# Kernel tuning notes

Hardware: AMD Instinct MI355X
Metric: run time of the kernel (lower is better)

## Reference

```python
import jax, jax.numpy as jnp
import numpy as np

D_MODEL = 1024
N_HEADS = 16
HEAD_DIM = D_MODEL // N_HEADS


def setup_inputs() -> dict:
    key = jax.random.key(0)
    ks = jax.random.split(key, 12)
    B, L = 2, 2048
    s = 1.0 / np.sqrt(D_MODEL)
    inp = {
        "q": jax.random.normal(ks[0], (B, L, D_MODEL), dtype=jnp.float32),
        "k": jax.random.normal(ks[1], (B, L, D_MODEL), dtype=jnp.float32),
        "v": jax.random.normal(ks[2], (B, L, D_MODEL), dtype=jnp.float32),
        "mask": jax.random.randint(ks[3], (B, L), 0, 2).astype(jnp.bool_),
        "Wq": jax.random.normal(ks[4], (D_MODEL, D_MODEL), dtype=jnp.float32) * s,
        "bq": jnp.zeros((D_MODEL,), dtype=jnp.float32),
        "Wk": jax.random.normal(ks[5], (D_MODEL, D_MODEL), dtype=jnp.float32) * s,
        "bk": jnp.zeros((D_MODEL,), dtype=jnp.float32),
        "Wv": jax.random.normal(ks[6], (D_MODEL, D_MODEL), dtype=jnp.float32) * s,
        "bv": jnp.zeros((D_MODEL,), dtype=jnp.float32),
        "Wo": jax.random.normal(ks[7], (D_MODEL, D_MODEL), dtype=jnp.float32) * s,
        "bo": jnp.zeros((D_MODEL,), dtype=jnp.float32),
    }
    return inp


def reference(q, k, v, mask, Wq, bq, Wk, bk, Wv, bv, Wo, bo):
    B, Lq, _ = q.shape
    Lk = k.shape[1]
    # torch Linear: y = x @ W.T + b; W is [out, in]
    Q = (jnp.einsum("bld,ed->ble", q, Wq) + bq).reshape(B, Lq, N_HEADS, HEAD_DIM).transpose(0, 2, 1, 3)
    K = (jnp.einsum("bld,ed->ble", k, Wk) + bk).reshape(B, Lk, N_HEADS, HEAD_DIM).transpose(0, 2, 1, 3)
    V = (jnp.einsum("bld,ed->ble", v, Wv) + bv).reshape(B, Lk, N_HEADS, HEAD_DIM).transpose(0, 2, 1, 3)
    scale = 1.0 / np.sqrt(HEAD_DIM).astype(np.float32)
    scores = jnp.einsum("bhqd,bhkd->bhqk", Q, K) * scale  # [B,H,Lq,Lk]
    # mask: True = masked out; broadcast (B,1,1,Lk)
    scores = jnp.where(mask[:, None, None, :], -jnp.inf, scores)
    attn = jax.nn.softmax(scores, axis=-1)
    out = jnp.einsum("bhqk,bhkd->bhqd", attn, V)  # [B,H,Lq,hd]
    out = out.transpose(0, 2, 1, 3).reshape(B, Lq, D_MODEL)
    return jnp.einsum("bld,ed->ble", out, Wo) + bo
```

## Files before the change

### kernel.cpp

```cpp
#include <hip/hip_runtime.h>

typedef unsigned short u16;
typedef __bf16 bf16x8 __attribute__((ext_vector_type(8)));
typedef float f32x4 __attribute__((ext_vector_type(4)));
typedef unsigned int u32x4 __attribute__((ext_vector_type(4)));
typedef unsigned int u32x2 __attribute__((ext_vector_type(2)));

#define MFMA16(a, b, c) __builtin_amdgcn_mfma_f32_16x16x32_bf16((a), (b), (c), 0, 0, 0)

__device__ __forceinline__ u16 f2bf(float f) {
    unsigned u = __builtin_bit_cast(unsigned, f);
    u = u + 0x7FFFu + ((u >> 16) & 1u);
    return (u16)(u >> 16);
}
__device__ __forceinline__ unsigned pk2(float a, float b) {
    return (unsigned)f2bf(a) | ((unsigned)f2bf(b) << 16);
}
__device__ __forceinline__ u32x4 pk8(f32x4 a, f32x4 b) {
    u32x4 r;
    r[0] = pk2(a[0], a[1]); r[1] = pk2(a[2], a[3]);
    r[2] = pk2(b[0], b[1]); r[3] = pk2(b[2], b[3]);
    return r;
}
__device__ __forceinline__ unsigned pkhu(float a, float b) {
    unsigned ua = __builtin_bit_cast(unsigned, a) + 0x8000u;
    unsigned ub = __builtin_bit_cast(unsigned, b) + 0x8000u;
    return __builtin_amdgcn_perm(ub, ua, 0x07060302u);
}
__device__ __forceinline__ float exp2_fast(float x) {
    float r;
    asm("v_exp_f32 %0, %1" : "=v"(r) : "v"(x));
    return r;
}
__device__ __forceinline__ void lds_load16(const u16* g, u16* l) {
    __builtin_amdgcn_global_load_lds(
        (const __attribute__((address_space(1))) void*)g,
        (__attribute__((address_space(3))) void*)l, 16, 0, 0);
}

#define QSCALE 0.18033688011112042f
#define FIXMAX 13.0f

__global__ __launch_bounds__(256) void convert_bf16(
    const float* __restrict__ q, const float* __restrict__ k, const float* __restrict__ v,
    const float* __restrict__ Wq, const float* __restrict__ Wk, const float* __restrict__ Wv,
    const float* __restrict__ Wo, u16* __restrict__ dst)
{
    const size_t i = ((size_t)blockIdx.x * 256 + threadIdx.x) * 8;
    const size_t QE = 4194304, WE = 1048576;
    const float* s;
    if (i < QE) s = q + i;
    else if (i < 2 * QE) s = k + (i - QE);
    else if (i < 3 * QE) s = v + (i - 2 * QE);
    else {
        size_t j = i - 3 * QE;
        if (j < WE) s = Wq + j;
        else if (j < 2 * WE) s = Wk + (j - WE);
        else if (j < 3 * WE) s = Wv + (j - 2 * WE);
        else s = Wo + (j - 3 * WE);
    }
    f32x4 a = *(const f32x4*)s;
    f32x4 b = *(const f32x4*)(s + 4);
    *(u32x4*)(dst + i) = pk8(a, b);
}

__device__ __forceinline__ void gemm128_core64(
    const u16* __restrict__ A, const u16* __restrict__ B,
    int m0, int n0, u16* As, u16* Bs, int tid, f32x4 acc[4][4])
{
    const int wv = tid >> 6, lane = tid & 63, quad = lane >> 4, l16 = lane & 15;
    const int mh = (wv >> 1) * 64, nh = (wv & 1) * 64;

    int rr[4], gc[4];
    u16 *ldsA[4], *ldsB[4];
    #pragma unroll
    for (int i = 0; i < 4; i++) {
        const int sbase = wv * 64 + i * 256;
        const int seg = sbase + lane;
        rr[i] = seg >> 3;
        const int c = seg & 7;
        gc[i] = c ^ (rr[i] & 7);
        ldsA[i] = As + sbase * 8;
        ldsB[i] = Bs + sbase * 8;
    }
    const u16* gA = A + (size_t)m0 * 1024;
    const u16* gB = B + (size_t)n0 * 1024;

    for (int t = 0; t < 16; t++) {
        const int k0 = t * 64;
        __syncthreads();
        #pragma unroll
        for (int i = 0; i < 4; i++)
            lds_load16(gA + (size_t)rr[i] * 1024 + k0 + gc[i] * 8, ldsA[i]);
        #pragma unroll
        for (int i = 0; i < 4; i++)
            lds_load16(gB + (size_t)rr[i] * 1024 + k0 + gc[i] * 8, ldsB[i]);
        __syncthreads();
        #pragma unroll
        for (int hf = 0; hf < 2; hf++) {
            bf16x8 af[4], bfr[4];
            #pragma unroll
            for (int mi = 0; mi < 4; mi++)
                af[mi] = *(const bf16x8*)&As[(mh + mi * 16 + l16) * 64 +
                                            (((quad + 4 * hf) ^ (l16 & 7)) * 8)];
            #pragma unroll
            for (int ni = 0; ni < 4; ni++)
                bfr[ni] = *(const bf16x8*)&Bs[(nh + ni * 16 + l16) * 64 +
                                              (((quad + 4 * hf) ^ (l16 & 7)) * 8)];
            #pragma unroll
            for (int mi = 0; mi < 4; mi++)
                #pragma unroll
                for (int ni = 0; ni < 4; ni++)
                    acc[mi][ni] = MFMA16(af[mi], bfr[ni], acc[mi][ni]);
        }
    }
}

__global__ __launch_bounds__(256) void qkv_bf(
    const u16* __restrict__ qb, const u16* __restrict__ kb, const u16* __restrict__ vb,
    const u16* __restrict__ wq, const u16* __restrict__ wk, const u16* __restrict__ wvv,
    const float* __restrict__ bq, const float* __restrict__ bk, const float* __restrict__ bv,
    u16* __restrict__ Qh, u16* __restrict__ Kh, u16* __restrict__ Vt)
{
    __shared__ alignas(16) u16 As[128 * 64];
    __shared__ alignas(16) u16 Bs[128 * 64];
    const int z = blockIdx.z;
    const u16* A = (z == 0) ? qb : (z == 1) ? kb : vb;
    const u16* B = (z == 0) ? wq : (z == 1) ? wk : wvv;
    const float* bias = (z == 0) ? bq : (z == 1) ? bk : bv;
    const int tid = threadIdx.x;
    const int m0 = blockIdx.y * 128, n0 = blockIdx.x * 128;
    const int wv = tid >> 6, lane = tid & 63, quad = lane >> 4, l16 = lane & 15;
    const int mh = (wv >> 1) * 64, nh = (wv & 1) * 64;

    f32x4 acc[4][4];
    #pragma unroll
    for (int i = 0; i < 4; i++)
        #pragma unroll
        for (int j = 0; j < 4; j++) acc[i][j] = (f32x4){0.f, 0.f, 0.f, 0.f};

    gemm128_core64(A, B, m0, n0, As, Bs, tid, acc);

    const float scl = (z == 0) ? QSCALE : 1.0f;
    u16* outp = (z == 0) ? Qh : (z == 1) ? Kh : Vt;
    #pragma unroll
    for (int ni = 0; ni < 4; ni++) {
        const int n = n0 + nh + ni * 16 + l16;
        const float bval = bias[n];
        const int h = n >> 6, d = n & 63;
        #pragma unroll
        for (int mi = 0; mi < 4; mi++) {
            const int mbase = m0 + mh + mi * 16 + quad * 4;
            #pragma unroll
            for (int r = 0; r < 4; r++) {
                const int m = mbase + r;
                const int bb = m >> 11, l = m & 2047;
                const float val = (acc[mi][ni][r] + bval) * scl;
                size_t idx;
                if (z < 2) idx = (((size_t)(bb * 16 + h) * 2048 + l) << 6) + d;
                else       idx = (((size_t)(bb * 16 + h) * 64 + d) << 11) + l;
                outp[idx] = f2bf(val);
            }
        }
    }
}

__global__ __launch_bounds__(256) void out_bf(
    const u16* __restrict__ Ob, const u16* __restrict__ wo,
    const float* __restrict__ bo, float* __restrict__ out)
{
    __shared__ alignas(16) u16 As[128 * 64];
    __shared__ alignas(16) u16 Bs[128 * 64];
    const int tid = threadIdx.x;
    const int m0 = blockIdx.y * 128, n0 = blockIdx.x * 128;
    const int wv = tid >> 6, lane = tid & 63, quad = lane >> 4, l16 = lane & 15;
    const int mh = (wv >> 1) * 64, nh = (wv & 1) * 64;

    f32x4 acc[4][4];
    #pragma unroll
    for (int i = 0; i < 4; i++)
        #pragma unroll
        for (int j = 0; j < 4; j++) acc[i][j] = (f32x4){0.f, 0.f, 0.f, 0.f};

    gemm128_core64(Ob, wo, m0, n0, As, Bs, tid, acc);

    #pragma unroll
    for (int ni = 0; ni < 4; ni++) {
        const int n = n0 + nh + ni * 16 + l16;
        const float bval = bo[n];
        #pragma unroll
        for (int mi = 0; mi < 4; mi++) {
            const int mbase = m0 + mh + mi * 16 + quad * 4;
            #pragma unroll
            for (int r = 0; r < 4; r++)
                out[(size_t)(mbase + r) * 1024 + n] = acc[mi][ni][r] + bval;
        }
    }
}

__global__ __launch_bounds__(256) void attn3(
    const u16* __restrict__ Qh, const u16* __restrict__ Kh,
    const u16* __restrict__ Vt, const int* __restrict__ mask,
    u16* __restrict__ Ob)
{
    __shared__ alignas(16) u16 Ks[2][64 * 72];
    __shared__ alignas(16) u16 Vs[2][64 * 72];
    __shared__ alignas(16) u16 Ps[4][16 * 72];
    __shared__ alignas(16) float Ms[2][64];

    const int tid = threadIdx.x;
    const int blk = blockIdx.x;
    const int bh = blk & 31, qt = blk >> 5;
    const int b = bh >> 4, h = bh & 15;
    const int wv = tid >> 6, lane = tid & 63, quad = lane >> 4, l16 = lane & 15;

    const int qbase = qt * 128 + wv * 32;
    const u16* Qb = Qh + ((size_t)bh * 2048 + qbase) * 64;
    bf16x8 qf[2][2];
    #pragma unroll
    for (int sub = 0; sub < 2; sub++)
        #pragma unroll
        for (int hf = 0; hf < 2; hf++)
            qf[sub][hf] = *(const bf16x8*)(Qb + (sub * 16 + l16) * 64 + hf * 32 + quad * 8);

    const u16* Kb = Kh + (size_t)bh * 2048 * 64;
    const u16* Vb = Vt + (size_t)bh * 64 * 2048;
    const int* mb = mask + b * 2048;

    const int s0 = tid, s1 = tid + 256;
    const int r0 = s0 >> 3, c0 = (s0 & 7) * 8;
    const int r1 = s1 >> 3, c1 = (s1 & 7) * 8;

    u32x4 rk0 = *(const u32x4*)(Kb + r0 * 64 + c0);
    u32x4 rk1 = *(const u32x4*)(Kb + r1 * 64 + c1);
    u32x4 rv0 = *(const u32x4*)(Vb + (size_t)r0 * 2048 + c0);
    u32x4 rv1 = *(const u32x4*)(Vb + (size_t)r1 * 2048 + c1);
    float rm = (tid < 64) ? (mb[tid] ? -1e30f : -FIXMAX) : 0.f;

    f32x4 o[2][4];
    #pragma unroll
    for (int sub = 0; sub < 2; sub++)
        #pragma unroll
        for (int db = 0; db < 4; db++) o[sub][db] = (f32x4){0.f, 0.f, 0.f, 0.f};
    float Lrun[2] = {0.f, 0.f};

    for (int kc = 0; kc < 32; kc++) {
        const int bi = kc & 1;
        u16* KsB = Ks[bi];
        u16* VsB = Vs[bi];
        *(u32x4*)&KsB[r0 * 72 + c0] = rk0;
        *(u32x4*)&KsB[r1 * 72 + c1] = rk1;
        *(u32x4*)&VsB[r0 * 72 + c0] = rv0;
        *(u32x4*)&VsB[r1 * 72 + c1] = rv1;
        if (tid < 64) Ms[bi][tid] = rm;
        __syncthreads();

        if (kc < 31) {
            const int off = (kc + 1) * 64;
            rk0 = *(const u32x4*)(Kb + (size_t)(off + r0) * 64 + c0);
            rk1 = *(const u32x4*)(Kb + (size_t)(off + r1) * 64 + c1);
            rv0 = *(const u32x4*)(Vb + (size_t)r0 * 2048 + off + c0);
            rv1 = *(const u32x4*)(Vb + (size_t)r1 * 2048 + off + c1);
            rm = (tid < 64) ? (mb[off + tid] ? -1e30f : -FIXMAX) : 0.f;
        }

        f32x4 mneg[4];
        #pragma unroll
        for (int nb = 0; nb < 4; nb++)
            mneg[nb] = *(const f32x4*)&Ms[bi][nb * 16 + quad * 4];

        #pragma unroll
        for (int sub = 0; sub < 2; sub++) {
            f32x4 st[4];
            #pragma unroll
            for (int nb = 0; nb < 4; nb++) {
                const bf16x8 kf0 = *(const bf16x8*)&KsB[(nb * 16 + l16) * 72 + quad * 8];
                const bf16x8 kf1 = *(const bf16x8*)&KsB[(nb * 16 + l16) * 72 + 32 + quad * 8];
                f32x4 z = (f32x4){0.f, 0.f, 0.f, 0.f};
                z = MFMA16(kf0, qf[sub][0], z);
                z = MFMA16(kf1, qf[sub][1], z);
                st[nb] = z;
            }
            #pragma unroll
            for (int nb = 0; nb < 4; nb++) {
                st[nb] += mneg[nb];
                #pragma unroll
                for (int r = 0; r < 4; r++) st[nb][r] = exp2_fast(st[nb][r]);
            }
            f32x4 s4 = st[0] + st[1] + st[2] + st[3];
            float sm = (s4[0] + s4[1]) + (s4[2] + s4[3]);
            sm += __shfl_xor(sm, 16, 64);
            sm += __shfl_xor(sm, 32, 64);
            Lrun[sub] += sm;

            u16* prow = &Ps[wv][l16 * 72];
            #pragma unroll
            for (int nb = 0; nb < 4; nb++) {
                u32x2 w;
                w[0] = pkhu(st[nb][0], st[nb][1]);
                w[1] = pkhu(st[nb][2], st[nb][3]);
                *(u32x2*)&prow[nb * 16 + quad * 4] = w;
            }

            asm volatile("s_waitcnt lgkmcnt(0)" ::: "memory");

            const bf16x8 pf0 = *(const bf16x8*)&Ps[wv][l16 * 72 + quad * 8];
            const bf16x8 pf1 = *(const bf16x8*)&Ps[wv][l16 * 72 + 32 + quad * 8];
            #pragma unroll
            for (int db = 0; db < 4; db++) {
                const bf16x8 vf0 = *(const bf16x8*)&VsB[(db * 16 + l16) * 72 + quad * 8];
                const bf16x8 vf1 = *(const bf16x8*)&VsB[(db * 16 + l16) * 72 + 32 + quad * 8];
                o[sub][db] = MFMA16(pf0, vf0, o[sub][db]);
                o[sub][db] = MFMA16(pf1, vf1, o[sub][db]);
            }
            asm volatile("" ::: "memory");
        }
    }

    #pragma unroll
    for (int sub = 0; sub < 2; sub++) {
        const float li = 1.0f / Lrun[sub];
        #pragma unroll
        for (int r = 0; r < 4; r++) {
            const float lr = __shfl(li, (lane & 48) | (quad * 4 + r), 64);
            const int qrow = qt * 128 + wv * 32 + sub * 16 + quad * 4 + r;
            #pragma unroll
            for (int db = 0; db < 4; db++)
                Ob[((size_t)(b * 2048 + qrow)) * 1024 + h * 64 + db * 16 + l16] =
                    f2bf(o[sub][db][r] * lr);
        }
    }
}

__global__ __launch_bounds__(256) void qkv_gemm(
    const float* __restrict__ q, const float* __restrict__ k, const float* __restrict__ v,
    const float* __restrict__ Wq, const float* __restrict__ Wk, const float* __restrict__ Wv,
    const float* __restrict__ bq, const float* __restrict__ bk, const float* __restrict__ bv,
    u16* __restrict__ Qh, u16* __restrict__ Kh, u16* __restrict__ Vt)
{
    __shared__ alignas(16) u16 As[128 * 40];
    __shared__ alignas(16) u16 Bs[128 * 40];
    const int z = blockIdx.z;
    const float* A    = (z == 0) ? q  : (z == 1) ? k  : v;
    const float* W    = (z == 0) ? Wq : (z == 1) ? Wk : Wv;
    const float* bias = (z == 0) ? bq : (z == 1) ? bk : bv;
    const int tid = threadIdx.x;
    const int m0 = blockIdx.y * 128, n0 = blockIdx.x * 128;
    const int row = tid >> 1, cseg = tid & 1;
    const float* ga = A + (size_t)(m0 + row) * 1024 + cseg * 16;
    const float* gb = W + (size_t)(n0 + row) * 1024 + cseg * 16;
    const int wv = tid >> 6, lane = tid & 63, quad = lane >> 4, l16 = lane & 15;
    const int mh = (wv >> 1) * 64, nh = (wv & 1) * 64;

    f32x4 acc[4][4];
    for (int i = 0; i < 4; i++)
        for (int j = 0; j < 4; j++) acc[i][j] = (f32x4){0.f, 0.f, 0.f, 0.f};

    f32x4 ra[4], rb[4];
    for (int i = 0; i < 4; i++) {
        ra[i] = *(const f32x4*)(ga + i * 4);
        rb[i] = *(const f32x4*)(gb + i * 4);
    }
    for (int t = 0; t < 32; t++) {
        __syncthreads();
        *(u32x4*)&As[row * 40 + cseg * 16]     = pk8(ra[0], ra[1]);
        *(u32x4*)&As[row * 40 + cseg * 16 + 8] = pk8(ra[2], ra[3]);
        *(u32x4*)&Bs[row * 40 + cseg * 16]     = pk8(rb[0], rb[1]);
        *(u32x4*)&Bs[row * 40 + cseg * 16 + 8] = pk8(rb[2], rb[3]);
        __syncthreads();
        if (t < 31) {
            const int k0 = (t + 1) * 32;
            for (int i = 0; i < 4; i++) {
                ra[i] = *(const f32x4*)(ga + k0 + i * 4);
                rb[i] = *(const f32x4*)(gb + k0 + i * 4);
            }
        }
        bf16x8 af[4], bfr[4];
        for (int mi = 0; mi < 4; mi++)
            af[mi] = *(const bf16x8*)&As[(mh + mi * 16 + l16) * 40 + quad * 8];
        for (int ni = 0; ni < 4; ni++)
            bfr[ni] = *(const bf16x8*)&Bs[(nh + ni * 16 + l16) * 40 + quad * 8];
        for (int mi = 0; mi < 4; mi++)
            for (int ni = 0; ni < 4; ni++)
                acc[mi][ni] = MFMA16(af[mi], bfr[ni], acc[mi][ni]);
    }
    const float scl = (z == 0) ? QSCALE : 1.0f;
    u16* outp = (z == 0) ? Qh : (z == 1) ? Kh : Vt;
    for (int ni = 0; ni < 4; ni++) {
        const int n = n0 + nh + ni * 16 + l16;
        const float bval = bias[n];
        const int h = n >> 6, d = n & 63;
        for (int mi = 0; mi < 4; mi++) {
            const int mbase = m0 + mh + mi * 16 + quad * 4;
            for (int r = 0; r < 4; r++) {
                const int m = mbase + r;
                const int bb = m >> 11, l = m & 2047;
                const float val = (acc[mi][ni][r] + bval) * scl;
                size_t idx;
                if (z < 2) idx = (((size_t)(bb * 16 + h) * 2048 + l) << 6) + d;
                else       idx = (((size_t)(bb * 16 + h) * 64 + d) << 11) + l;
                outp[idx] = f2bf(val);
            }
        }
    }
}

__global__ __launch_bounds__(256) void out_gemm(
    const u16* __restrict__ Ob, const float* __restrict__ Wo,
    const float* __restrict__ bo, float* __restrict__ out)
{
    __shared__ alignas(16) u16 As[128 * 40];
    __shared__ alignas(16) u16 Bs[128 * 40];
    const int tid = threadIdx.x;
    const int m0 = blockIdx.y * 128, n0 = blockIdx.x * 128;
    const int row = tid >> 1, cseg = tid & 1;
    const u16* ga = Ob + (size_t)(m0 + row) * 1024 + cseg * 16;
    const float* gb = Wo + (size_t)(n0 + row) * 1024 + cseg * 16;
    const int wv = tid >> 6, lane = tid & 63, quad = lane >> 4, l16 = lane & 15;
    const int mh = (wv >> 1) * 64, nh = (wv & 1) * 64;

    f32x4 acc[4][4];
    for (int i = 0; i < 4; i++)
        for (int j = 0; j < 4; j++) acc[i][j] = (f32x4){0.f, 0.f, 0.f, 0.f};

    u32x4 ra0 = *(const u32x4*)(ga);
    u32x4 ra1 = *(const u32x4*)(ga + 8);
    f32x4 rb[4];
    for (int i = 0; i < 4; i++) rb[i] = *(const f32x4*)(gb + i * 4);

    for (int t = 0; t < 32; t++) {
        __syncthreads();
        *(u32x4*)&As[row * 40 + cseg * 16]     = ra0;
        *(u32x4*)&As[row * 40 + cseg * 16 + 8] = ra1;
        *(u32x4*)&Bs[row * 40 + cseg * 16]     = pk8(rb[0], rb[1]);
        *(u32x4*)&Bs[row * 40 + cseg * 16 + 8] = pk8(rb[2], rb[3]);
        __syncthreads();
        if (t < 31) {
            const int k0 = (t + 1) * 32;
            ra0 = *(const u32x4*)(ga + k0);
            ra1 = *(const u32x4*)(ga + k0 + 8);
            for (int i = 0; i < 4; i++) rb[i] = *(const f32x4*)(gb + k0 + i * 4);
        }
        bf16x8 af[4], bfr[4];
        for (int mi = 0; mi < 4; mi++)
            af[mi] = *(const bf16x8*)&As[(mh + mi * 16 + l16) * 40 + quad * 8];
        for (int ni = 0; ni < 4; ni++)
            bfr[ni] = *(const bf16x8*)&Bs[(nh + ni * 16 + l16) * 40 + quad * 8];
        for (int mi = 0; mi < 4; mi++)
            for (int ni = 0; ni < 4; ni++)
                acc[mi][ni] = MFMA16(af[mi], bfr[ni], acc[mi][ni]);
    }
    for (int ni = 0; ni < 4; ni++) {
        const int n = n0 + nh + ni * 16 + l16;
        const float bval = bo[n];
        for (int mi = 0; mi < 4; mi++) {
            const int mbase = m0 + mh + mi * 16 + quad * 4;
            for (int r = 0; r < 4; r++)
                out[(size_t)(mbase + r) * 1024 + n] = acc[mi][ni][r] + bval;
        }
    }
}

extern "C" void kernel_launch(void* const* d_in, const int* in_sizes, int n_in,
                              void* d_out, int out_size, void* d_ws, size_t ws_size,
                              hipStream_t stream)
{
    (void)in_sizes; (void)n_in; (void)out_size;
    const float* q  = (const float*)d_in[0];
    const float* k  = (const float*)d_in[1];
    const float* v  = (const float*)d_in[2];
    const int* mask = (const int*)d_in[3];
    const float* Wq = (const float*)d_in[4];
    const float* bq = (const float*)d_in[5];
    const float* Wk = (const float*)d_in[6];
    const float* bk = (const float*)d_in[7];
    const float* Wv = (const float*)d_in[8];
    const float* bv = (const float*)d_in[9];
    const float* Wo = (const float*)d_in[10];
    const float* bo = (const float*)d_in[11];
    float* out = (float*)d_out;

    u16* ws = (u16*)d_ws;
    const size_t QE = 4194304, WE = 1048576;
    const size_t NEED = (6 * QE + 4 * WE) * 2;

    if (ws_size >= NEED) {
        u16* qbf = ws;
        u16* kbf = ws + QE;
        u16* vbf = ws + 2 * QE;
        u16* wqb = ws + 3 * QE;
        u16* wkb = wqb + WE;
        u16* wvb = wqb + 2 * WE;
        u16* wob = wqb + 3 * WE;
        u16* Qh  = ws + 3 * QE + 4 * WE;
        u16* Kh  = Qh + QE;
        u16* Vth = Qh + 2 * QE;
        u16* Obp = qbf;
        convert_bf16<<<dim3(8192), 256, 0, stream>>>(q, k, v, Wq, Wk, Wv, Wo, ws);
        qkv_bf<<<dim3(8, 32, 3), 256, 0, stream>>>(qbf, kbf, vbf, wqb, wkb, wvb,
                                                   bq, bk, bv, Qh, Kh, Vth);
        attn3<<<dim3(512), 256, 0, stream>>>(Qh, Kh, Vth, mask, Obp);
        out_bf<<<dim3(8, 32), 256, 0, stream>>>(Obp, wob, bo, out);
    } else {
        u16* Qh  = ws;
        u16* Kh  = ws + QE;
        u16* Vth = ws + 2 * QE;
        u16* Obp = ws + 3 * QE;
        qkv_gemm<<<dim3(8, 32, 3), 256, 0, stream>>>(q, k, v, Wq, Wk, Wv,
                                                     bq, bk, bv, Qh, Kh, Vth);
        attn3<<<dim3(512), 256, 0, stream>>>(Qh, Kh, Vth, mask, Obp);
        out_gemm<<<dim3(8, 32), 256, 0, stream>>>(Obp, Wo, bo, out);
    }
}
```

Before: 262.6 us.

## Shrink GEMM K-tile, stage QKV epilogue through LDS, halve attention query tile

The GEMM core switches from 64-wide swizzled K tiles to 32-wide unswizzled tiles, which halves LDS use and doubles the number of barrier iterations. The QKV epilogue now writes results into shared memory and then emits coalesced 16-byte global stores, instead of scattered 2-byte stores. The attention kernel processes 16 query rows per wave instead of 32 and launches twice as many blocks, trading K/V reuse for more parallelism and lower register pressure. The unswizzled 32-wide LDS layout may cause bank conflicts on the fragment reads.

Result: slower. 278.6 us (+6.1%).

```diff
diff --git a/kernel.cpp b/kernel.cpp
--- a/kernel.cpp
+++ b/kernel.cpp
@@ -1,6 +1,7 @@
 #include <hip/hip_runtime.h>
 
 typedef unsigned short u16;
+typedef unsigned long long u64;
 typedef __bf16 bf16x8 __attribute__((ext_vector_type(8)));
 typedef float f32x4 __attribute__((ext_vector_type(4)));
 typedef unsigned int u32x4 __attribute__((ext_vector_type(4)));
@@ -64,55 +65,43 @@
     *(u32x4*)(dst + i) = pk8(a, b);
 }
 
-__device__ __forceinline__ void gemm128_core64(
+__device__ __forceinline__ void gemm128_core(
     const u16* __restrict__ A, const u16* __restrict__ B,
     int m0, int n0, u16* As, u16* Bs, int tid, f32x4 acc[4][4])
 {
     const int wv = tid >> 6, lane = tid & 63, quad = lane >> 4, l16 = lane & 15;
     const int mh = (wv >> 1) * 64, nh = (wv & 1) * 64;
-
-    int rr[4], gc[4];
-    u16 *ldsA[4], *ldsB[4];
-    #pragma unroll
-    for (int i = 0; i < 4; i++) {
-        const int sbase = wv * 64 + i * 256;
-        const int seg = sbase + lane;
-        rr[i] = seg >> 3;
-        const int c = seg & 7;
-        gc[i] = c ^ (rr[i] & 7);
-        ldsA[i] = As + sbase * 8;
-        ldsB[i] = Bs + sbase * 8;
-    }
+    const int segA0 = wv * 128 + lane;
+    const int segA1 = wv * 128 + 64 + lane;
+    const int ra0 = segA0 >> 2, ca0 = (segA0 & 3) * 8;
+    const int ra1 = segA1 >> 2, ca1 = (segA1 & 3) * 8;
+    u16* ldsA0 = &As[(wv * 128) * 8];
+    u16* ldsA1 = &As[(wv * 128 + 64) * 8];
+    u16* ldsB0 = &Bs[(wv * 128) * 8];
+    u16* ldsB1 = &Bs[(wv * 128 + 64) * 8];
     const u16* gA = A + (size_t)m0 * 1024;
     const u16* gB = B + (size_t)n0 * 1024;
 
-    for (int t = 0; t < 16; t++) {
-        const int k0 = t * 64;
-        __syncthreads();
-        #pragma unroll
-        for (int i = 0; i < 4; i++)
-            lds_load16(gA + (size_t)rr[i] * 1024 + k0 + gc[i] * 8, ldsA[i]);
-        #pragma unroll
-        for (int i = 0; i < 4; i++)
-            lds_load16(gB + (size_t)rr[i] * 1024 + k0 + gc[i] * 8, ldsB[i]);
-        __syncthreads();
-        #pragma unroll
-        for (int hf = 0; hf < 2; hf++) {
-            bf16x8 af[4], bfr[4];
-            #pragma unroll
-            for (int mi = 0; mi < 4; mi++)
-                af[mi] = *(const bf16x8*)&As[(mh + mi * 16 + l16) * 64 +
-                                            (((quad + 4 * hf) ^ (l16 & 7)) * 8)];
+    for (int t = 0; t < 32; t++) {
+        const int k0 = t * 32;
+        __syncthreads();
+        lds_load16(gA + (size_t)ra0 * 1024 + k0 + ca0, ldsA0);
+        lds_load16(gA + (size_t)ra1 * 1024 + k0 + ca1, ldsA1);
+        lds_load16(gB + (size_t)ra0 * 1024 + k0 + ca0, ldsB0);
+        lds_load16(gB + (size_t)ra1 * 1024 + k0 + ca1, ldsB1);
+        __syncthreads();
+        bf16x8 af[4], bfr[4];
+        #pragma unroll
+        for (int mi = 0; mi < 4; mi++)
+            af[mi] = *(const bf16x8*)&As[(mh + mi * 16 + l16) * 32 + quad * 8];
+        #pragma unroll
+        for (int ni = 0; ni < 4; ni++)
+            bfr[ni] = *(const bf16x8*)&Bs[(nh + ni * 16 + l16) * 32 + quad * 8];
+        #pragma unroll
+        for (int mi = 0; mi < 4; mi++)
             #pragma unroll
             for (int ni = 0; ni < 4; ni++)
-                bfr[ni] = *(const bf16x8*)&Bs[(nh + ni * 16 + l16) * 64 +
-                                              (((quad + 4 * hf) ^ (l16 & 7)) * 8)];
-            #pragma unroll
-            for (int mi = 0; mi < 4; mi++)
-                #pragma unroll
-                for (int ni = 0; ni < 4; ni++)
-                    acc[mi][ni] = MFMA16(af[mi], bfr[ni], acc[mi][ni]);
-        }
+                acc[mi][ni] = MFMA16(af[mi], bfr[ni], acc[mi][ni]);
     }
 }
 
@@ -122,8 +111,10 @@
     const float* __restrict__ bq, const float* __restrict__ bk, const float* __restrict__ bv,
     u16* __restrict__ Qh, u16* __restrict__ Kh, u16* __restrict__ Vt)
 {
-    __shared__ alignas(16) u16 As[128 * 64];
-    __shared__ alignas(16) u16 Bs[128 * 64];
+    __shared__ alignas(16) u16 SH[8192];
+    u16* As = SH;
+    u16* Bs = SH + 4096;
+
     const int z = blockIdx.z;
     const u16* A = (z == 0) ? qb : (z == 1) ? kb : vb;
     const u16* B = (z == 0) ? wq : (z == 1) ? wk : wvv;
@@ -139,28 +130,74 @@
         #pragma unroll
         for (int j = 0; j < 4; j++) acc[i][j] = (f32x4){0.f, 0.f, 0.f, 0.f};
 
-    gemm128_core64(A, B, m0, n0, As, Bs, tid, acc);
+    gemm128_core(A, B, m0, n0, As, Bs, tid, acc);
 
     const float scl = (z == 0) ? QSCALE : 1.0f;
     u16* outp = (z == 0) ? Qh : (z == 1) ? Kh : Vt;
-    #pragma unroll
-    for (int ni = 0; ni < 4; ni++) {
-        const int n = n0 + nh + ni * 16 + l16;
-        const float bval = bias[n];
-        const int h = n >> 6, d = n & 63;
-        #pragma unroll
-        for (int mi = 0; mi < 4; mi++) {
-            const int mbase = m0 + mh + mi * 16 + quad * 4;
-            #pragma unroll
-            for (int r = 0; r < 4; r++) {
-                const int m = mbase + r;
-                const int bb = m >> 11, l = m & 2047;
-                const float val = (acc[mi][ni][r] + bval) * scl;
-                size_t idx;
-                if (z < 2) idx = (((size_t)(bb * 16 + h) * 2048 + l) << 6) + d;
-                else       idx = (((size_t)(bb * 16 + h) * 64 + d) << 11) + l;
-                outp[idx] = f2bf(val);
+    const int h0 = n0 >> 6;
+    const int bb = m0 >> 11, l0 = m0 & 2047;
+
+    #pragma unroll
+    for (int p = 0; p < 2; p++) {
+        __syncthreads();
+        if (z < 2) {
+            if ((mh >> 6) == p) {
+                #pragma unroll
+                for (int ni = 0; ni < 4; ni++) {
+                    const int n = n0 + nh + ni * 16 + l16;
+                    const float bval = bias[n];
+                    const int col = nh + ni * 16 + l16;
+                    #pragma unroll
+                    for (int mi = 0; mi < 4; mi++) {
+                        #pragma unroll
+                        for (int r = 0; r < 4; r++) {
+                            const int rr = mi * 16 + quad * 4 + r;
+                            const int cp = (((col >> 3) ^ (rr & 15)) << 3) | (col & 7);
+                            SH[rr * 128 + cp] = f2bf((acc[mi][ni][r] + bval) * scl);
+                        }
+                    }
+                }
             }
+        } else {
+            if ((nh >> 6) == p) {
+                #pragma unroll
+                for (int ni = 0; ni < 4; ni++) {
+                    const int n = n0 + nh + ni * 16 + l16;
+                    const float bval = bias[n];
+                    const int rr = ni * 16 + l16;
+                    #pragma unroll
+                    for (int mi = 0; mi < 4; mi++) {
+                        const int col = mh + mi * 16 + quad * 4;
+                        const int cp = (((col >> 3) ^ (rr & 15)) << 3) | (col & 7);
+                        u32x2 w;
+                        w[0] = pk2(acc[mi][ni][0] + bval, acc[mi][ni][1] + bval);
+                        w[1] = pk2(acc[mi][ni][2] + bval, acc[mi][ni][3] + bval);
+                        *(u32x2*)&SH[rr * 128 + cp] = w;
+                    }
+                }
+            }
+        }
+        __syncthreads();
+        const int rr = tid >> 2;
+        const int sb = (tid & 3) * 4;
+        #pragma unroll
+        for (int s = 0; s < 4; s++) {
+            const int seg = sb + s;
+            const int c = seg * 8;
+            const int cp = ((seg ^ (rr & 15)) << 3);
+            const u32x4 val = *(const u32x4*)&SH[rr * 128 + cp];
+            size_t gidx;
+            if (z < 2) {
+                const int m = m0 + p * 64 + rr;
+                const int l = m & 2047, bbb = m >> 11;
+                const int h = h0 + (c >> 6), d = c & 63;
+                gidx = (((size_t)(bbb * 16 + h) * 2048 + l) << 6) + d;
+            } else {
+                const int n = n0 + p * 64 + rr;
+                const int h = n >> 6, dd = n & 63;
+                gidx = (((size_t)(bb * 16 + h) * 64 + dd) << 11) + l0 + c;
+            }
+            *(u32x4*)&outp[gidx] = val;
         }
     }
 }
@@ -169,8 +206,9 @@
     const u16* __restrict__ Ob, const u16* __restrict__ wo,
     const float* __restrict__ bo, float* __restrict__ out)
 {
-    __shared__ alignas(16) u16 As[128 * 64];
-    __shared__ alignas(16) u16 Bs[128 * 64];
+    __shared__ alignas(16) u16 SH[8192];
+    u16* As = SH;
+    u16* Bs = SH + 4096;
     const int tid = threadIdx.x;
     const int m0 = blockIdx.y * 128, n0 = blockIdx.x * 128;
     const int wv = tid >> 6, lane = tid & 63, quad = lane >> 4, l16 = lane & 15;
@@ -182,7 +220,7 @@
         #pragma unroll
         for (int j = 0; j < 4; j++) acc[i][j] = (f32x4){0.f, 0.f, 0.f, 0.f};
 
-    gemm128_core64(Ob, wo, m0, n0, As, Bs, tid, acc);
+    gemm128_core(Ob, wo, m0, n0, As, Bs, tid, acc);
 
     #pragma unroll
     for (int ni = 0; ni < 4; ni++) {
@@ -198,7 +236,7 @@
     }
 }
 
-__global__ __launch_bounds__(256) void attn3(
+__global__ __launch_bounds__(256) void attn4(
     const u16* __restrict__ Qh, const u16* __restrict__ Kh,
     const u16* __restrict__ Vt, const int* __restrict__ mask,
     u16* __restrict__ Ob)
@@ -214,14 +252,12 @@
     const int b = bh >> 4, h = bh & 15;
     const int wv = tid >> 6, lane = tid & 63, quad = lane >> 4, l16 = lane & 15;
 
-    const int qbase = qt * 128 + wv * 32;
+    const int qbase = qt * 64 + wv * 16;
     const u16* Qb = Qh + ((size_t)bh * 2048 + qbase) * 64;
-    bf16x8 qf[2][2];
-    #pragma unroll
-    for (int sub = 0; sub < 2; sub++)
-        #pragma unroll
-        for (int hf = 0; hf < 2; hf++)
-            qf[sub][hf] = *(const bf16x8*)(Qb + (sub * 16 + l16) * 64 + hf * 32 + quad * 8);
+    bf16x8 qf[2];
+    #pragma unroll
+    for (int hf = 0; hf < 2; hf++)
+        qf[hf] = *(const bf16x8*)(Qb + l16 * 64 + hf * 32 + quad * 8);
 
     const u16* Kb = Kh + (size_t)bh * 2048 * 64;
     const u16* Vb = Vt + (size_t)bh * 64 * 2048;
@@ -237,12 +273,10 @@
     u32x4 rv1 = *(const u32x4*)(Vb + (size_t)r1 * 2048 + c1);
     float rm = (tid < 64) ? (mb[tid] ? -1e30f : -FIXMAX) : 0.f;
 
-    f32x4 o[2][4];
-    #pragma unroll
-    for (int sub = 0; sub < 2; sub++)
-        #pragma unroll
-        for (int db = 0; db < 4; db++) o[sub][db] = (f32x4){0.f, 0.f, 0.f, 0.f};
-    float Lrun[2] = {0.f, 0.f};
+    f32x4 o[4];
+    #pragma unroll
+    for (int db = 0; db < 4; db++) o[db] = (f32x4){0.f, 0.f, 0.f, 0.f};
+    float Lrun = 0.f;
 
     for (int kc = 0; kc < 32; kc++) {
         const int bi = kc & 1;
@@ -264,71 +298,59 @@
             rm = (tid < 64) ? (mb[off + tid] ? -1e30f : -FIXMAX) : 0.f;
         }
 
-        f32x4 mneg[4];
-        #pragma unroll
-        for (int nb = 0; nb < 4; nb++)
-            mneg[nb] = *(const f32x4*)&Ms[bi][nb * 16 + quad * 4];
-
-        #pragma unroll
-        for (int sub = 0; sub < 2; sub++) {
-            f32x4 st[4];
+        f32x4 st[4];
+        #pragma unroll
+        for (int nb = 0; nb < 4; nb++) {
+            const bf16x8 kf0 = *(const bf16x8*)&KsB[(nb * 16 + l16) * 72 + quad * 8];
+            const bf16x8 kf1 = *(const bf16x8*)&KsB[(nb * 16 + l16) * 72 + 32 + quad * 8];
+            f32x4 z = (f32x4){0.f, 0.f, 0.f, 0.f};
+            z = MFMA16(kf0, qf[0], z);
+            z = MFMA16(kf1, qf[1], z);
+            st[nb] = z;
+        }
+        #pragma unroll
+        for (int nb = 0; nb < 4; nb++) {
+            st[nb] += *(const f32x4*)&Ms[bi][nb * 16 + quad * 4];
             #pragma unroll
-            for (int nb = 0; nb < 4; nb++) {
-                const bf16x8 kf0 = *(const bf16x8*)&KsB[(nb * 16 + l16) * 72 + quad * 8];
-                const bf16x8 kf1 = *(const bf16x8*)&KsB[(nb * 16 + l16) * 72 + 32 + quad * 8];
-                f32x4 z = (f32x4){0.f, 0.f, 0.f, 0.f};
-                z = MFMA16(kf0, qf[sub][0], z);
-                z = MFMA16(kf1, qf[sub][1], z);
-                st[nb] = z;
-            }
-            #pragma unroll
-            for (int nb = 0; nb < 4; nb++) {
-                st[nb] += mneg[nb];
-                #pragma unroll
-                for (int r = 0; r < 4; r++) st[nb][r] = exp2_fast(st[nb][r]);
-            }
-            f32x4 s4 = st[0] + st[1] + st[2] + st[3];
-            float sm = (s4[0] + s4[1]) + (s4[2] + s4[3]);
-            sm += __shfl_xor(sm, 16, 64);
-            sm += __shfl_xor(sm, 32, 64);
-            Lrun[sub] += sm;
-
-            u16* prow = &Ps[wv][l16 * 72];
-            #pragma unroll
-            for (int nb = 0; nb < 4; nb++) {
-                u32x2 w;
-                w[0] = pkhu(st[nb][0], st[nb][1]);
-                w[1] = pkhu(st[nb][2], st[nb][3]);
-                *(u32x2*)&prow[nb * 16 + quad * 4] = w;
-            }
-
-            asm volatile("s_waitcnt lgkmcnt(0)" ::: "memory");
-
-            const bf16x8 pf0 = *(const bf16x8*)&Ps[wv][l16 * 72 + quad * 8];
-            const bf16x8 pf1 = *(const bf16x8*)&Ps[wv][l16 * 72 + 32 + quad * 8];
-            #pragma unroll
-            for (int db = 0; db < 4; db++) {
-                const bf16x8 vf0 = *(const bf16x8*)&VsB[(db * 16 + l16) * 72 + quad * 8];
-                const bf16x8 vf1 = *(const bf16x8*)&VsB[(db * 16 + l16) * 72 + 32 + quad * 8];
-                o[sub][db] = MFMA16(pf0, vf0, o[sub][db]);
-                o[sub][db] = MFMA16(pf1, vf1, o[sub][db]);
-            }
-            asm volatile("" ::: "memory");
-        }
-    }
-
-    #pragma unroll
-    for (int sub = 0; sub < 2; sub++) {
-        const float li = 1.0f / Lrun[sub];
-        #pragma unroll
-        for (int r = 0; r < 4; r++) {
-            const float lr = __shfl(li, (lane & 48) | (quad * 4 + r), 64);
-            const int qrow = qt * 128 + wv * 32 + sub * 16 + quad * 4 + r;
-            #pragma unroll
-            for (int db = 0; db < 4; db++)
-                Ob[((size_t)(b * 2048 + qrow)) * 1024 + h * 64 + db * 16 + l16] =
-                    f2bf(o[sub][db][r] * lr);
-        }
+            for (int r = 0; r < 4; r++) st[nb][r] = exp2_fast(st[nb][r]);
+        }
+        f32x4 s4 = (st[0] + st[1]) + (st[2] + st[3]);
+        float sm = (s4[0] + s4[1]) + (s4[2] + s4[3]);
+        sm += __shfl_xor(sm, 16, 64);
+        sm += __shfl_xor(sm, 32, 64);
+        Lrun += sm;
+
+        u16* prow = &Ps[wv][l16 * 72];
+        #pragma unroll
+        for (int nb = 0; nb < 4; nb++) {
+            u32x2 w;
+            w[0] = pkhu(st[nb][0], st[nb][1]);
+            w[1] = pkhu(st[nb][2], st[nb][3]);
+            *(u32x2*)&prow[nb * 16 + quad * 4] = w;
+        }
+        asm volatile("s_waitcnt lgkmcnt(0)" ::: "memory");
+
+        const bf16x8 pf0 = *(const bf16x8*)&Ps[wv][l16 * 72 + quad * 8];
+        const bf16x8 pf1 = *(const bf16x8*)&Ps[wv][l16 * 72 + 32 + quad * 8];
+        #pragma unroll
+        for (int db = 0; db < 4; db++) {
+            const bf16x8 vf0 = *(const bf16x8*)&VsB[(db * 16 + l16) * 72 + quad * 8];
+            const bf16x8 vf1 = *(const bf16x8*)&VsB[(db * 16 + l16) * 72 + 32 + quad * 8];
+            o[db] = MFMA16(pf0, vf0, o[db]);
+            o[db] = MFMA16(pf1, vf1, o[db]);
+        }
+        asm volatile("" ::: "memory");
+    }
+
+    const float li = 1.0f / Lrun;
+    #pragma unroll
+    for (int r = 0; r < 4; r++) {
+        const float lr = __shfl(li, (lane & 48) | (quad * 4 + r), 64);
+        const int qrow = qt * 64 + wv * 16 + quad * 4 + r;
+        #pragma unroll
+        for (int db = 0; db < 4; db++)
+            Ob[((size_t)(b * 2048 + qrow)) * 1024 + h * 64 + db * 16 + l16] =
+                f2bf(o[db][r] * lr);
     }
 }
 
@@ -499,7 +521,7 @@
         convert_bf16<<<dim3(8192), 256, 0, stream>>>(q, k, v, Wq, Wk, Wv, Wo, ws);
         qkv_bf<<<dim3(8, 32, 3), 256, 0, stream>>>(qbf, kbf, vbf, wqb, wkb, wvb,
                                                    bq, bk, bv, Qh, Kh, Vth);
-        attn3<<<dim3(512), 256, 0, stream>>>(Qh, Kh, Vth, mask, Obp);
+        attn4<<<dim3(1024), 256, 0, stream>>>(Qh, Kh, Vth, mask, Obp);
         out_bf<<<dim3(8, 32), 256, 0, stream>>>(Obp, wob, bo, out);
     } else {
         u16* Qh  = ws;
@@ -508,7 +530,7 @@
         u16* Obp = ws + 3 * QE;
         qkv_gemm<<<dim3(8, 32, 3), 256, 0, stream>>>(q, k, v, Wq, Wk, Wv,
                                                      bq, bk, bv, Qh, Kh, Vth);
-        attn3<<<dim3(512), 256, 0, stream>>>(Qh, Kh, Vth, mask, Obp);
+        attn4<<<dim3(1024), 256, 0, stream>>>(Qh, Kh, Vth, mask, Obp);
         out_gemm<<<dim3(8, 32), 256, 0, stream>>>(Obp, Wo, bo, out);
     }
 }
```
